# Kernel tuning notes

Hardware: AMD Instinct MI355X
Metric: run time of the kernel (lower is better)

The kernel has to match this reference:

```python
import jax, jax.numpy as jnp
import numpy as np
import math

B, S, D = 2, 4096, 512
H, DH = 8, 64
L = 128            # num_landmarks
W = 128            # window_size
EXT = W // 2       # 64
WIN = 2 * EXT + W  # 256
G = S // W         # 32 chunks
EPS = 1e-5


def _ln(x, g, b):
    mu = jnp.mean(x, axis=-1, keepdims=True)
    var = jnp.mean((x - mu) ** 2, axis=-1, keepdims=True)
    return (x - mu) * jax.lax.rsqrt(var + EPS) * g + b


def setup_inputs() -> dict:
    key = jax.random.key(0)
    ks = jax.random.split(key, 12)
    sd = 1.0 / math.sqrt(D)
    inp = {
        "X": jax.random.normal(ks[0], (B, S, D), dtype=jnp.float32),
        "mask": jnp.ones((B, S), dtype=jnp.int32),
        "Wq": jax.random.normal(ks[1], (D, H * DH), dtype=jnp.float32) * sd,
        "bq": jnp.zeros((H * DH,), jnp.float32),
        "Wk": jax.random.normal(ks[2], (D, H * DH), dtype=jnp.float32) * sd,
        "bk": jnp.zeros((H * DH,), jnp.float32),
        "Wv": jax.random.normal(ks[3], (D, H * DH), dtype=jnp.float32) * sd,
        "bv": jnp.zeros((H * DH,), jnp.float32),
        "Wo": jax.random.normal(ks[4], (H * DH, D), dtype=jnp.float32) * sd,
        "bo": jnp.zeros((D,), jnp.float32),
        "ln_l_g": jnp.ones((H * DH,), jnp.float32),
        "ln_l_b": jnp.zeros((H * DH,), jnp.float32),
        "ln_s_g": jnp.ones((H * DH,), jnp.float32),
        "ln_s_b": jnp.zeros((H * DH,), jnp.float32),
        "Wd": jax.random.normal(ks[5], (D, H * L), dtype=jnp.float32) * sd,
        "bd": jnp.zeros((H * L,), jnp.float32),
    }
    return inp


def reference(X, mask, Wq, bq, Wk, bk, Wv, bv, Wo, bo,
              ln_l_g, ln_l_b, ln_s_g, ln_s_b, Wd, bd):
    scale = 1.0 / math.sqrt(DH)

    def split(x):  # [B,S,H*DH] -> [B,H,S,DH]
        return x.reshape(B, S, H, DH).transpose(0, 2, 1, 3)

    Q = split(X @ Wq + bq) * scale
    K = split(_ln(X @ Wk + bk, ln_l_g, ln_l_b))
    V = split(_ln(X @ Wv + bv, ln_l_g, ln_l_b))
    pad_mask = (mask == 0)  # True = padding, [B,S]

    # ---- landmark compression branch ----
    hs = jax.nn.softmax((X @ Wd + bd).astype(jnp.float32), axis=1)  # over seq
    hs = hs.astype(X.dtype).reshape(B, S, H, L).transpose(0, 2, 3, 1)  # [B,H,L,S]
    Kc = jnp.einsum('bhls,bhsd->bhld', hs, K)
    Vc = jnp.einsum('bhls,bhsd->bhld', hs, V)
    # dual_ln_s over full model dim
    Kc = _ln(Kc.transpose(0, 2, 1, 3).reshape(B, L, H * DH), ln_s_g, ln_s_b)
    Kc = Kc.reshape(B, L, H, DH).transpose(0, 2, 1, 3)
    Vc = _ln(Vc.transpose(0, 2, 1, 3).reshape(B, L, H * DH), ln_s_g, ln_s_b)
    Vc = Vc.reshape(B, L, H, DH).transpose(0, 2, 1, 3)

    attn_c = jnp.einsum('bhqd,bhld->bhql', Q, Kc)  # [B,H,S,L]

    # ---- sliding-window branch (v2 tiling) ----
    idx = jnp.arange(G)[:, None] * W + jnp.arange(WIN)[None, :]
    K_pad = jnp.pad(K, ((0, 0), (0, 0), (EXT, EXT), (0, 0)))
    K_tiles = K_pad[:, :, idx, :]
    Qt = Q.reshape(B, H, G, W, DH)
    win_scores = jnp.einsum('bhgqd,bhgkd->bhgqk', Qt, K_tiles)
    mask_pad = jnp.pad(pad_mask, ((0, 0), (EXT, EXT)), constant_values=True)
    mask_tiles = mask_pad[:, idx]
    win_scores = jnp.where(mask_tiles[:, None, :, None, :], -jnp.inf, win_scores)
    win_scores = win_scores.reshape(B, H, S, WIN)

    # ---- joint softmax over [landmarks | window] ----
    all_scores = jnp.concatenate([attn_c, win_scores], axis=-1)
    all_attn = jax.nn.softmax(all_scores.astype(jnp.float32), axis=-1).astype(X.dtype)
    all_attn = jnp.where(pad_mask[:, None, :, None], 0.0, all_attn)

    C = jnp.einsum('bhql,bhld->bhqd', all_attn[..., :L], Vc)
    wp = all_attn[..., L:].reshape(B, H, G, W, WIN)
    V_pad = jnp.pad(V, ((0, 0), (0, 0), (EXT, EXT), (0, 0)))
    V_tiles = V_pad[:, :, idx, :]
    C = C + jnp.einsum('bhgqk,bhgkd->bhgqd', wp, V_tiles).reshape(B, H, S, DH)

    out = C.transpose(0, 2, 1, 3).reshape(B, S, H * DH) @ Wo + bo
    return out
```

## Files before the change

kernel.cpp:

```cpp
#include <hip/hip_runtime.h>
#include <hip/hip_bf16.h>

#define S_LEN 4096
#define Hn 8
#define DHn 64
#define Lc 128
#define HL 1024
#define KD 512

typedef __attribute__((ext_vector_type(8))) short bshort8;
typedef __attribute__((ext_vector_type(4))) float f32x4;

__device__ __forceinline__ short f2bs(float f) {
    union { float f; unsigned u; } x; x.f = f;
    const unsigned r = x.u + 0x7FFFu + ((x.u >> 16) & 1u);
    return (short)(r >> 16);
}
__device__ __forceinline__ float bs2f(short s) {
    union { unsigned u; float f; } x; x.u = ((unsigned)(unsigned short)s) << 16;
    return x.f;
}

__device__ __forceinline__ void gl16(const short* g, short* l) {
    __builtin_amdgcn_global_load_lds((const __attribute__((address_space(1))) void*)g,
                                     (__attribute__((address_space(3))) void*)l, 16, 0, 0);
}

__global__ __launch_bounds__(256) void prep_all(const float* __restrict__ X,
    const float* __restrict__ Wq, const float* __restrict__ Wk, const float* __restrict__ Wv,
    const float* __restrict__ Wd, const float* __restrict__ Wo,
    short* __restrict__ Xbf, short* __restrict__ WTall, short* __restrict__ WoT)
{
    const int t = threadIdx.x;
    int blk = blockIdx.x;
    if (blk < 2048) {
        const int i = (blk * 256 + t) * 8;
        const float4 a = *(const float4*)&X[i];
        const float4 b = *(const float4*)&X[i + 4];
        bshort8 o;
        o[0] = f2bs(a.x); o[1] = f2bs(a.y); o[2] = f2bs(a.z); o[3] = f2bs(a.w);
        o[4] = f2bs(b.x); o[5] = f2bs(b.y); o[6] = f2bs(b.z); o[7] = f2bs(b.w);
        *(bshort8*)&Xbf[i] = o;
        return;
    }
    blk -= 2048;
    const float* W; short* out; int N;
    if (blk < 256)       { W = Wq; out = WTall;              N = 512;  }
    else if (blk < 512)  { W = Wk; out = WTall + 512 * 512;  N = 512;  blk -= 256; }
    else if (blk < 768)  { W = Wv; out = WTall + 1024 * 512; N = 512;  blk -= 512; }
    else if (blk < 1280) { W = Wd; out = WTall + 1536 * 512; N = 1024; blk -= 768; }
    else                 { W = Wo; out = WoT;                N = 512;  blk -= 1280; }
    const int nb = N >> 5;
    const int n0 = (blk % nb) * 32, k0 = (blk / nb) * 32;
    __shared__ float Tl[32][33];
    const int tx = t & 31, ty = t >> 5;
#pragma unroll
    for (int i = ty; i < 32; i += 8)
        Tl[i][tx] = W[(size_t)(k0 + i) * N + n0 + tx];
    __syncthreads();
#pragma unroll
    for (int i = ty; i < 32; i += 8)
        out[(size_t)(n0 + i) * KD + k0 + tx] = f2bs(Tl[tx][i]);
}

__global__ __launch_bounds__(256) void gemm_proj(const short* __restrict__ Xbf,
    const short* __restrict__ WT,
    const float* __restrict__ bq, const float* __restrict__ bk,
    const float* __restrict__ bv, const float* __restrict__ bd,
    short* __restrict__ Qbf, short* __restrict__ KbBf, short* __restrict__ VbBf,
    short* __restrict__ DlogBf)
{
    __shared__ __align__(16) short A_s[128 * 32];
    __shared__ __align__(16) short B_s[128 * 32];
    const int t = threadIdx.x;
    const int n0 = blockIdx.x * 128, m0 = blockIdx.y * 128;
    const int lane = t & 63, wave = t >> 6;
    const int wm = wave >> 1, wn = wave & 1;
    const int quad = lane >> 4, r15 = lane & 15;
    const int eOff = t * 8;
    const int am = eOff >> 5, ak = eOff & 31;
    f32x4 acc[4][4];
#pragma unroll
    for (int i = 0; i < 4; ++i)
#pragma unroll
        for (int j = 0; j < 4; ++j) acc[i][j] = (f32x4){0.f, 0.f, 0.f, 0.f};

    for (int kk = 0; kk < KD; kk += 32) {
        gl16(&Xbf[(size_t)(m0 + am) * KD + kk + ak],      &A_s[eOff]);
        gl16(&Xbf[(size_t)(m0 + 64 + am) * KD + kk + ak], &A_s[2048 + eOff]);
        gl16(&WT[(size_t)(n0 + am) * KD + kk + ak],       &B_s[eOff]);
        gl16(&WT[(size_t)(n0 + 64 + am) * KD + kk + ak],  &B_s[2048 + eOff]);
        __syncthreads();
        bshort8 af[4], bfr[4];
#pragma unroll
        for (int i = 0; i < 4; ++i) af[i]  = *(const bshort8*)&A_s[(wm * 64 + i * 16 + r15) * 32 + quad * 8];
#pragma unroll
        for (int j = 0; j < 4; ++j) bfr[j] = *(const bshort8*)&B_s[(wn * 64 + j * 16 + r15) * 32 + quad * 8];
#pragma unroll
        for (int i = 0; i < 4; ++i)
#pragma unroll
            for (int j = 0; j < 4; ++j)
                acc[i][j] = __builtin_amdgcn_mfma_f32_16x16x32_bf16(af[i], bfr[j], acc[i][j], 0, 0, 0);
        __syncthreads();
    }
    const int seg = (n0 >= 1536) ? 3 : (n0 >> 9);
#pragma unroll
    for (int i = 0; i < 4; ++i)
#pragma unroll
        for (int j = 0; j < 4; ++j)
#pragma unroll
            for (int r = 0; r < 4; ++r) {
                const int gm = m0 + wm * 64 + i * 16 + quad * 4 + r;
                const int gn = n0 + wn * 64 + j * 16 + r15;
                float v = acc[i][j][r];
                if (seg == 0) {
                    v = (v + bq[gn]) * 0.125f;
                    const int bb = gm >> 12, s = gm & 4095, hh = gn >> 6, d = gn & 63;
                    Qbf[((size_t)(bb * Hn + hh) * S_LEN + s) * DHn + d] = f2bs(v);
                } else if (seg == 1) {
                    KbBf[(size_t)gm * 512 + (gn - 512)] = f2bs(v + bk[gn - 512]);
                } else if (seg == 2) {
                    VbBf[(size_t)gm * 512 + (gn - 1024)] = f2bs(v + bv[gn - 1024]);
                } else {
                    DlogBf[(size_t)gm * 1024 + (gn - 1536)] = f2bs(v + bd[gn - 1536]);
                }
            }
}

__global__ __launch_bounds__(256) void gemm_out(const short* __restrict__ Abf,
    const short* __restrict__ WT, const float* __restrict__ bias, float* __restrict__ outp)
{
    __shared__ __align__(16) short A_s[64 * 32];
    __shared__ __align__(16) short B_s[64 * 32];
    const int t = threadIdx.x;
    const int n0 = blockIdx.x * 64, m0 = blockIdx.y * 64;
    const int lane = t & 63, wave = t >> 6;
    const int quad = lane >> 4, r15 = lane & 15;
    const int eOff = t * 8;
    const int am = eOff >> 5, ak = eOff & 31;
    f32x4 acc[4];
#pragma unroll
    for (int j = 0; j < 4; ++j) acc[j] = (f32x4){0.f, 0.f, 0.f, 0.f};

    for (int kk = 0; kk < KD; kk += 32) {
        gl16(&Abf[(size_t)(m0 + am) * KD + kk + ak], &A_s[eOff]);
        gl16(&WT[(size_t)(n0 + am) * KD + kk + ak],  &B_s[eOff]);
        __syncthreads();
        const bshort8 af = *(const bshort8*)&A_s[(wave * 16 + r15) * 32 + quad * 8];
#pragma unroll
        for (int j = 0; j < 4; ++j) {
            const bshort8 bfr = *(const bshort8*)&B_s[(j * 16 + r15) * 32 + quad * 8];
            acc[j] = __builtin_amdgcn_mfma_f32_16x16x32_bf16(af, bfr, acc[j], 0, 0, 0);
        }
        __syncthreads();
    }
#pragma unroll
    for (int j = 0; j < 4; ++j)
#pragma unroll
        for (int r = 0; r < 4; ++r) {
            const int gm = m0 + wave * 16 + quad * 4 + r;
            const int gn = n0 + j * 16 + r15;
            outp[(size_t)gm * 512 + gn] = acc[j][r] + bias[gn];
        }
}

__global__ __launch_bounds__(256) void ln_ip(const short* __restrict__ KbBf, const short* __restrict__ VbBf,
    const float* __restrict__ g, const float* __restrict__ beta,
    short* __restrict__ Kbf, short* __restrict__ Vbf)
{
    const short* src = blockIdx.y ? VbBf : KbBf;
    short* dst = blockIdx.y ? Vbf : Kbf;
    const int row = blockIdx.x, t = threadIdx.x;
    const size_t base = (size_t)row * 512;
    const float x0 = bs2f(src[base + t]);
    const float x1 = bs2f(src[base + t + 256]);
    float s = x0 + x1, ss = x0 * x0 + x1 * x1;
#pragma unroll
    for (int off = 32; off >= 1; off >>= 1) { s += __shfl_xor(s, off); ss += __shfl_xor(ss, off); }
    __shared__ float red[2][4];
    if ((t & 63) == 0) { red[0][t >> 6] = s; red[1][t >> 6] = ss; }
    __syncthreads();
    s = red[0][0] + red[0][1] + red[0][2] + red[0][3];
    ss = red[1][0] + red[1][1] + red[1][2] + red[1][3];
    const float mu = s * (1.f / 512.f);
    const float r = rsqrtf(ss * (1.f / 512.f) - mu * mu + 1e-5f);
    const int bb = row >> 12, sidx = row & 4095;
#pragma unroll
    for (int half = 0; half < 2; ++half) {
        const int c = t + half * 256;
        const float x = half ? x1 : x0;
        const float v = (x - mu) * r * g[c] + beta[c];
        dst[((size_t)(bb * Hn + (c >> 6)) * S_LEN + sidx) * DHn + (c & 63)] = f2bs(v);
    }
}

__global__ __launch_bounds__(256) void kcvc_mfma(const short* __restrict__ Dlog,
    const short* __restrict__ Kbf, const short* __restrict__ Vbf,
    short* __restrict__ partK, short* __restrict__ partV, float* __restrict__ partZ)
{
    __shared__ __align__(16) short aa[128 * 72];
    __shared__ __align__(16) short Kt[64 * 72];
    __shared__ __align__(16) short Vt[64 * 72];
    __shared__ float zsh[256];
    const int t = threadIdx.x;
    const int seg = blockIdx.x, h = blockIdx.y, b = blockIdx.z;
    const int s0 = seg * 128;
    const size_t bh = (size_t)(b * Hn + h);
    const int lane = t & 63, wave = t >> 6;
    const int quad = lane >> 4, r15 = lane & 15;
    const int al = t & 127, ah = t >> 7;
    const int vj = t & 63, vd0 = (t >> 6) * 16;
    float zacc = 0.f;
    f32x4 aK[2][4], aV[2][4];
#pragma unroll
    for (int i = 0; i < 2; ++i)
#pragma unroll
        for (int j = 0; j < 4; ++j) { aK[i][j] = (f32x4){0.f,0.f,0.f,0.f}; aV[i][j] = (f32x4){0.f,0.f,0.f,0.f}; }

    for (int c = 0; c < 2; ++c) {
        const int sc0 = s0 + c * 64;
        if (c) __syncthreads();
#pragma unroll
        for (int gch = 0; gch < 4; ++gch) {
            bshort8 o;
#pragma unroll
            for (int j = 0; j < 8; ++j) {
                const int s = sc0 + ah * 32 + gch * 8 + j;
                const float e = __expf(bs2f(Dlog[((size_t)b * S_LEN + s) * HL + h * Lc + al]));
                zacc += e;
                o[j] = f2bs(e);
            }
            *(bshort8*)&aa[al * 72 + ah * 32 + gch * 8] = o;
        }
        {
            const size_t rb = (bh * S_LEN + sc0 + vj) * DHn + vd0;
            const bshort8 k0 = *(const bshort8*)&Kbf[rb];
            const bshort8 k1 = *(const bshort8*)&Kbf[rb + 8];
            const bshort8 v0 = *(const bshort8*)&Vbf[rb];
            const bshort8 v1 = *(const bshort8*)&Vbf[rb + 8];
#pragma unroll
            for (int i = 0; i < 8; ++i) {
                Kt[(vd0 + i) * 72 + vj] = k0[i]; Kt[(vd0 + 8 + i) * 72 + vj] = k1[i];
                Vt[(vd0 + i) * 72 + vj] = v0[i]; Vt[(vd0 + 8 + i) * 72 + vj] = v1[i];
            }
        }
        __syncthreads();
#pragma unroll
        for (int ks = 0; ks < 2; ++ks) {
            const bshort8 a0 = *(const bshort8*)&aa[(wave * 32 + r15) * 72 + ks * 32 + quad * 8];
            const bshort8 a1 = *(const bshort8*)&aa[(wave * 32 + 16 + r15) * 72 + ks * 32 + quad * 8];
#pragma unroll
            for (int j = 0; j < 4; ++j) {
                const bshort8 bk = *(const bshort8*)&Kt[(j * 16 + r15) * 72 + ks * 32 + quad * 8];
                const bshort8 bv = *(const bshort8*)&Vt[(j * 16 + r15) * 72 + ks * 32 + quad * 8];
                aK[0][j] = __builtin_amdgcn_mfma_f32_16x16x32_bf16(a0, bk, aK[0][j], 0, 0, 0);
                aK[1][j] = __builtin_amdgcn_mfma_f32_16x16x32_bf16(a1, bk, aK[1][j], 0, 0, 0);
                aV[0][j] = __builtin_amdgcn_mfma_f32_16x16x32_bf16(a0, bv, aV[0][j], 0, 0, 0);
                aV[1][j] = __builtin_amdgcn_mfma_f32_16x16x32_bf16(a1, bv, aV[1][j], 0, 0, 0);
            }
        }
    }
    zsh[t] = zacc;
    __syncthreads();
    if (t < 128)
        partZ[((size_t)(bh * Lc + t)) * 32 + seg] = zsh[t] + zsh[t + 128];
#pragma unroll
    for (int i = 0; i < 2; ++i)
#pragma unroll
        for (int j = 0; j < 4; ++j)
#pragma unroll
            for (int r = 0; r < 4; ++r) {
                const int l = wave * 32 + i * 16 + quad * 4 + r;
                const int d = j * 16 + r15;
                const size_t o = (((size_t)(b * Lc + l)) * 32 + seg) * 512 + h * 64 + d;
                partK[o] = f2bs(aK[i][j][r]);
                partV[o] = f2bs(aV[i][j][r]);
            }
}

__global__ __launch_bounds__(256) void kcvc_s2(const short* __restrict__ partK,
    const short* __restrict__ partV, const float* __restrict__ partZ,
    const float* __restrict__ g, const float* __restrict__ beta,
    short* __restrict__ KcBf, short* __restrict__ VcBf)
{
    const int l = blockIdx.x, b = blockIdx.y, t = threadIdx.x;
    __shared__ float zh[8];
    if (t < 8) {
        float z = 0.f;
        const size_t zb = ((size_t)((b * Hn + t) * Lc + l)) * 32;
#pragma unroll
        for (int seg = 0; seg < 32; ++seg) z += partZ[zb + seg];
        zh[t] = 1.f / z;
    }
    const size_t base = ((size_t)(b * Lc + l)) * 32 * 512;
    float k0 = 0.f, k1 = 0.f, v0 = 0.f, v1 = 0.f;
    for (int ch = 0; ch < 32; ++ch) {
        const size_t o = base + (size_t)ch * 512;
        k0 += bs2f(partK[o + t]);       k1 += bs2f(partK[o + t + 256]);
        v0 += bs2f(partV[o + t]);       v1 += bs2f(partV[o + t + 256]);
    }
    __syncthreads();
    const float z0 = zh[t >> 6], z1 = zh[(t + 256) >> 6];
    k0 *= z0; k1 *= z1; v0 *= z0; v1 *= z1;
    float sk = k0 + k1, ssk = k0 * k0 + k1 * k1;
    float sv = v0 + v1, ssv = v0 * v0 + v1 * v1;
#pragma unroll
    for (int off = 32; off >= 1; off >>= 1) {
        sk += __shfl_xor(sk, off); ssk += __shfl_xor(ssk, off);
        sv += __shfl_xor(sv, off); ssv += __shfl_xor(ssv, off);
    }
    __shared__ float red[4][4];
    if ((t & 63) == 0) {
        red[0][t >> 6] = sk; red[1][t >> 6] = ssk;
        red[2][t >> 6] = sv; red[3][t >> 6] = ssv;
    }
    __syncthreads();
    sk = red[0][0] + red[0][1] + red[0][2] + red[0][3];
    ssk = red[1][0] + red[1][1] + red[1][2] + red[1][3];
    sv = red[2][0] + red[2][1] + red[2][2] + red[2][3];
    ssv = red[3][0] + red[3][1] + red[3][2] + red[3][3];
    const float muK = sk * (1.f / 512.f);
    const float rK = rsqrtf(ssk * (1.f / 512.f) - muK * muK + 1e-5f);
    const float muV = sv * (1.f / 512.f);
    const float rV = rsqrtf(ssv * (1.f / 512.f) - muV * muV + 1e-5f);
#pragma unroll
    for (int half = 0; half < 2; ++half) {
        const int c = t + half * 256;
        const float xk = half ? k1 : k0;
        const float xv = half ? v1 : v0;
        const size_t o = ((size_t)(b * Hn + (c >> 6)) * Lc + l) * DHn + (c & 63);
        KcBf[o] = f2bs((xk - muK) * rK * g[c] + beta[c]);
        VcBf[o] = f2bs((xv - muV) * rV * g[c] + beta[c]);
    }
}

__global__ __launch_bounds__(256) void attn_mfma(
    const short* __restrict__ Qbf, const short* __restrict__ Kbf, const short* __restrict__ Vbf,
    const short* __restrict__ KcBf, const short* __restrict__ VcBf,
    const int* __restrict__ mask, short* __restrict__ C)
{
    __shared__ __align__(16) short Q_l[128 * 72];
    __shared__ __align__(16) short K_l[64 * 72];
    __shared__ __align__(16) short Vt_l[64 * 72];
    __shared__ __align__(16) short P_l[128 * 72];
    __shared__ float vb[64];
    const int t = threadIdx.x;
    const int qt = blockIdx.x, h = blockIdx.y, b = blockIdx.z;
    const int q0 = qt * 128;
    const size_t bh = (size_t)(b * Hn + h);
    const int lane = t & 63, wave = t >> 6;
    const int quad = lane >> 4, r15 = lane & 15;
    const int sr = t >> 2, sc = (t & 3) * 16;
    const int vj = t & 63, vd0 = (t >> 6) * 16;

#pragma unroll
    for (int r = 0; r < 2; ++r) {
        const int row = r * 64 + sr;
        const size_t gq = (bh * S_LEN + q0 + row) * DHn + sc;
        const bshort8 a = *(const bshort8*)&Qbf[gq];
        const bshort8 b8 = *(const bshort8*)&Qbf[gq + 8];
        *(bshort8*)&Q_l[row * 72 + sc] = a;
        *(bshort8*)&Q_l[row * 72 + sc + 8] = b8;
    }
    f32x4 o[2][4];
#pragma unroll
    for (int i = 0; i < 2; ++i)
#pragma unroll
        for (int df = 0; df < 4; ++df) o[i][df] = (f32x4){0.f, 0.f, 0.f, 0.f};
    float lrow[2][4] = {{0.f, 0.f, 0.f, 0.f}, {0.f, 0.f, 0.f, 0.f}};

    for (int cc = 0; cc < 6; ++cc) {
        const short* ksrc; const short* vsrc;
        int sk0 = 0;
        if (cc < 2) {
            ksrc = &KcBf[(bh * Lc + cc * 64) * DHn];
            vsrc = &VcBf[(bh * Lc + cc * 64) * DHn];
        } else {
            sk0 = q0 - 64 + (cc - 2) * 64;
            if (sk0 < 0 || sk0 >= S_LEN) continue;
            ksrc = &Kbf[(bh * S_LEN + sk0) * DHn];
            vsrc = &Vbf[(bh * S_LEN + sk0) * DHn];
        }
        __syncthreads();
        if (t < 64) {
            float v = 0.f;
            if (cc >= 2 && mask[b * S_LEN + sk0 + t] == 0) v = -1e30f;
            vb[t] = v;
        }
        {
            const bshort8 a = *(const bshort8*)&ksrc[sr * 64 + sc];
            const bshort8 b8 = *(const bshort8*)&ksrc[sr * 64 + sc + 8];
            *(bshort8*)&K_l[sr * 72 + sc] = a;
            *(bshort8*)&K_l[sr * 72 + sc + 8] = b8;
        }
        {
            const bshort8 v0 = *(const bshort8*)&vsrc[vj * 64 + vd0];
            const bshort8 v1 = *(const bshort8*)&vsrc[vj * 64 + vd0 + 8];
#pragma unroll
            for (int i = 0; i < 8; ++i) {
                Vt_l[(vd0 + i) * 72 + vj] = v0[i];
                Vt_l[(vd0 + 8 + i) * 72 + vj] = v1[i];
            }
        }
        __syncthreads();
        f32x4 c[2][4];
#pragma unroll
        for (int i = 0; i < 2; ++i)
#pragma unroll
            for (int jf = 0; jf < 4; ++jf) c[i][jf] = (f32x4){0.f, 0.f, 0.f, 0.f};
#pragma unroll
        for (int ks = 0; ks < 2; ++ks) {
            bshort8 aq[2];
#pragma unroll
            for (int i = 0; i < 2; ++i)
                aq[i] = *(const bshort8*)&Q_l[(wave * 32 + i * 16 + r15) * 72 + ks * 32 + quad * 8];
#pragma unroll
            for (int jf = 0; jf < 4; ++jf) {
                const bshort8 bk = *(const bshort8*)&K_l[(jf * 16 + r15) * 72 + ks * 32 + quad * 8];
                c[0][jf] = __builtin_amdgcn_mfma_f32_16x16x32_bf16(aq[0], bk, c[0][jf], 0, 0, 0);
                c[1][jf] = __builtin_amdgcn_mfma_f32_16x16x32_bf16(aq[1], bk, c[1][jf], 0, 0, 0);
            }
        }
        float vbl[4];
#pragma unroll
        for (int jf = 0; jf < 4; ++jf) vbl[jf] = vb[jf * 16 + r15];
        float sum[2][4] = {{0.f, 0.f, 0.f, 0.f}, {0.f, 0.f, 0.f, 0.f}};
#pragma unroll
        for (int i = 0; i < 2; ++i)
#pragma unroll
            for (int jf = 0; jf < 4; ++jf)
#pragma unroll
                for (int r = 0; r < 4; ++r) {
                    const float p = __expf(c[i][jf][r] + vbl[jf]);
                    sum[i][r] += p;
                    P_l[(wave * 32 + i * 16 + quad * 4 + r) * 72 + jf * 16 + r15] = f2bs(p);
                }
#pragma unroll
        for (int off = 1; off <= 8; off <<= 1)
#pragma unroll
            for (int i = 0; i < 2; ++i)
#pragma unroll
                for (int r = 0; r < 4; ++r) sum[i][r] += __shfl_xor(sum[i][r], off);
#pragma unroll
        for (int i = 0; i < 2; ++i)
#pragma unroll
            for (int r = 0; r < 4; ++r) lrow[i][r] += sum[i][r];
#pragma unroll
        for (int ks = 0; ks < 2; ++ks) {
            bshort8 ap[2];
#pragma unroll
            for (int i = 0; i < 2; ++i)
                ap[i] = *(const bshort8*)&P_l[(wave * 32 + i * 16 + r15) * 72 + ks * 32 + quad * 8];
#pragma unroll
            for (int df = 0; df < 4; ++df) {
                const bshort8 bv = *(const bshort8*)&Vt_l[(df * 16 + r15) * 72 + ks * 32 + quad * 8];
                o[0][df] = __builtin_amdgcn_mfma_f32_16x16x32_bf16(ap[0], bv, o[0][df], 0, 0, 0);
                o[1][df] = __builtin_amdgcn_mfma_f32_16x16x32_bf16(ap[1], bv, o[1][df], 0, 0, 0);
            }
        }
    }
#pragma unroll
    for (int i = 0; i < 2; ++i)
#pragma unroll
        for (int r = 0; r < 4; ++r) {
            const int q = q0 + wave * 32 + i * 16 + quad * 4 + r;
            const float rl = (mask[b * S_LEN + q] == 0) ? 0.f : (1.f / lrow[i][r]);
            const size_t ob = ((size_t)b * S_LEN + q) * 512 + h * 64;
#pragma unroll
            for (int df = 0; df < 4; ++df)
                C[ob + df * 16 + r15] = f2bs(o[i][df][r] * rl);
        }
}

extern "C" void kernel_launch(void* const* d_in, const int* in_sizes, int n_in,
                              void* d_out, int out_size, void* d_ws, size_t ws_size,
                              hipStream_t stream) {
    (void)in_sizes; (void)n_in; (void)out_size; (void)ws_size;
    const float* X    = (const float*)d_in[0];
    const int*   mask = (const int*)d_in[1];
    const float* Wq = (const float*)d_in[2];  const float* bq = (const float*)d_in[3];
    const float* Wk = (const float*)d_in[4];  const float* bk = (const float*)d_in[5];
    const float* Wv = (const float*)d_in[6];  const float* bv = (const float*)d_in[7];
    const float* Wo = (const float*)d_in[8];  const float* bo = (const float*)d_in[9];
    const float* lnlg = (const float*)d_in[10]; const float* lnlb = (const float*)d_in[11];
    const float* lnsg = (const float*)d_in[12]; const float* lnsb = (const float*)d_in[13];
    const float* Wd = (const float*)d_in[14]; const float* bd = (const float*)d_in[15];

    short* sw = (short*)d_ws;
    short* Qbf    = sw;
    short* Kbf    = Qbf + 4194304;
    short* Vbf    = Kbf + 4194304;
    short* KbBf   = Vbf + 4194304;
    short* VbBf   = KbBf + 4194304;
    short* DlogBf = VbBf + 4194304;
    short* Xbf    = DlogBf + 8388608;
    short* WTall  = Xbf + 4194304;
    short* WoT    = WTall + 1310720;
    short* KcBf   = WoT + 262144;
    short* VcBf   = KcBf + 131072;
    short* partV  = VcBf + 131072;
    float* partZ  = (float*)(partV + 4194304);
    short* partK  = Xbf;
    short* Cbf    = Xbf;

    const dim3 blk(256);
    prep_all<<<3584, blk, 0, stream>>>(X, Wq, Wk, Wv, Wd, Wo, Xbf, WTall, WoT);
    gemm_proj<<<dim3(20, 64), blk, 0, stream>>>(Xbf, WTall, bq, bk, bv, bd, Qbf, KbBf, VbBf, DlogBf);
    ln_ip<<<dim3(8192, 2), blk, 0, stream>>>(KbBf, VbBf, lnlg, lnlb, Kbf, Vbf);
    kcvc_mfma<<<dim3(32, 8, 2), blk, 0, stream>>>(DlogBf, Kbf, Vbf, partK, partV, partZ);
    kcvc_s2<<<dim3(128, 2), blk, 0, stream>>>(partK, partV, partZ, lnsg, lnsb, KcBf, VcBf);
    attn_mfma<<<dim3(32, 8, 2), blk, 0, stream>>>(Qbf, Kbf, Vbf, KcBf, VcBf, mask, Cbf);
    gemm_out<<<dim3(8, 128), blk, 0, stream>>>(Cbf, WoT, bo, (float*)d_out);
}
```

Baseline: 220.9 us.

## Remap GEMM block order for XCD locality, widen out-proj tile, split kcvc_s2 by K/V

The projection and output GEMMs now use a 1D grid whose block index is remapped so that consecutive blocks landing on the same XCD (id & 7) share output column tiles, aiming to improve L2 reuse of weight and activation tiles. The output GEMM tile is widened from 64x64 to 64x128, giving each wave 8 accumulators and halving redundant A loads at the cost of more registers and fewer blocks. kcvc_s2 is split across a z-dimension so K and V are normalized by separate blocks, doubling parallelism for that small reduction kernel but recomputing the Z normalizers twice.

Measured after the change: 210.7 us. -4.6%, faster.

```diff
diff --git a/kernel.cpp b/kernel.cpp
--- a/kernel.cpp
+++ b/kernel.cpp
@@ -73,7 +73,10 @@
     __shared__ __align__(16) short A_s[128 * 32];
     __shared__ __align__(16) short B_s[128 * 32];
     const int t = threadIdx.x;
-    const int n0 = blockIdx.x * 128, m0 = blockIdx.y * 128;
+    const int id = blockIdx.x;
+    const int x8 = id & 7, j8 = id >> 3;
+    const int m0 = (x8 * 8 + (j8 & 7)) * 128;
+    const int n0 = (j8 >> 3) * 128;
     const int lane = t & 63, wave = t >> 6;
     const int wm = wave >> 1, wn = wave & 1;
     const int quad = lane >> 4, r15 = lane & 15;
@@ -131,31 +134,35 @@
     const short* __restrict__ WT, const float* __restrict__ bias, float* __restrict__ outp)
 {
     __shared__ __align__(16) short A_s[64 * 32];
-    __shared__ __align__(16) short B_s[64 * 32];
+    __shared__ __align__(16) short B_s[128 * 32];
     const int t = threadIdx.x;
-    const int n0 = blockIdx.x * 64, m0 = blockIdx.y * 64;
+    const int id = blockIdx.x;
+    const int x8 = id & 7, j8 = id >> 3;
+    const int m0 = (x8 * 16 + (j8 & 15)) * 64;
+    const int n0 = (j8 >> 4) * 128;
     const int lane = t & 63, wave = t >> 6;
     const int quad = lane >> 4, r15 = lane & 15;
     const int eOff = t * 8;
     const int am = eOff >> 5, ak = eOff & 31;
-    f32x4 acc[4];
-#pragma unroll
-    for (int j = 0; j < 4; ++j) acc[j] = (f32x4){0.f, 0.f, 0.f, 0.f};
+    f32x4 acc[8];
+#pragma unroll
+    for (int j = 0; j < 8; ++j) acc[j] = (f32x4){0.f, 0.f, 0.f, 0.f};
 
     for (int kk = 0; kk < KD; kk += 32) {
-        gl16(&Abf[(size_t)(m0 + am) * KD + kk + ak], &A_s[eOff]);
-        gl16(&WT[(size_t)(n0 + am) * KD + kk + ak],  &B_s[eOff]);
+        gl16(&Abf[(size_t)(m0 + am) * KD + kk + ak],      &A_s[eOff]);
+        gl16(&WT[(size_t)(n0 + am) * KD + kk + ak],       &B_s[eOff]);
+        gl16(&WT[(size_t)(n0 + 64 + am) * KD + kk + ak],  &B_s[2048 + eOff]);
         __syncthreads();
         const bshort8 af = *(const bshort8*)&A_s[(wave * 16 + r15) * 32 + quad * 8];
 #pragma unroll
-        for (int j = 0; j < 4; ++j) {
+        for (int j = 0; j < 8; ++j) {
             const bshort8 bfr = *(const bshort8*)&B_s[(j * 16 + r15) * 32 + quad * 8];
             acc[j] = __builtin_amdgcn_mfma_f32_16x16x32_bf16(af, bfr, acc[j], 0, 0, 0);
         }
         __syncthreads();
     }
 #pragma unroll
-    for (int j = 0; j < 4; ++j)
+    for (int j = 0; j < 8; ++j)
 #pragma unroll
         for (int r = 0; r < 4; ++r) {
             const int gm = m0 + wave * 16 + quad * 4 + r;
@@ -284,6 +291,8 @@
     short* __restrict__ KcBf, short* __restrict__ VcBf)
 {
     const int l = blockIdx.x, b = blockIdx.y, t = threadIdx.x;
+    const short* part = blockIdx.z ? partV : partK;
+    short* dst = blockIdx.z ? VcBf : KcBf;
     __shared__ float zh[8];
     if (t < 8) {
         float z = 0.f;
@@ -293,44 +302,33 @@
         zh[t] = 1.f / z;
     }
     const size_t base = ((size_t)(b * Lc + l)) * 32 * 512;
-    float k0 = 0.f, k1 = 0.f, v0 = 0.f, v1 = 0.f;
+    float k0 = 0.f, k1 = 0.f;
     for (int ch = 0; ch < 32; ++ch) {
         const size_t o = base + (size_t)ch * 512;
-        k0 += bs2f(partK[o + t]);       k1 += bs2f(partK[o + t + 256]);
-        v0 += bs2f(partV[o + t]);       v1 += bs2f(partV[o + t + 256]);
+        k0 += bs2f(part[o + t]);
+        k1 += bs2f(part[o + t + 256]);
     }
     __syncthreads();
     const float z0 = zh[t >> 6], z1 = zh[(t + 256) >> 6];
-    k0 *= z0; k1 *= z1; v0 *= z0; v1 *= z1;
+    k0 *= z0; k1 *= z1;
     float sk = k0 + k1, ssk = k0 * k0 + k1 * k1;
-    float sv = v0 + v1, ssv = v0 * v0 + v1 * v1;
 #pragma unroll
     for (int off = 32; off >= 1; off >>= 1) {
         sk += __shfl_xor(sk, off); ssk += __shfl_xor(ssk, off);
-        sv += __shfl_xor(sv, off); ssv += __shfl_xor(ssv, off);
-    }
-    __shared__ float red[4][4];
-    if ((t & 63) == 0) {
-        red[0][t >> 6] = sk; red[1][t >> 6] = ssk;
-        red[2][t >> 6] = sv; red[3][t >> 6] = ssv;
-    }
+    }
+    __shared__ float red[2][4];
+    if ((t & 63) == 0) { red[0][t >> 6] = sk; red[1][t >> 6] = ssk; }
     __syncthreads();
     sk = red[0][0] + red[0][1] + red[0][2] + red[0][3];
     ssk = red[1][0] + red[1][1] + red[1][2] + red[1][3];
-    sv = red[2][0] + red[2][1] + red[2][2] + red[2][3];
-    ssv = red[3][0] + red[3][1] + red[3][2] + red[3][3];
-    const float muK = sk * (1.f / 512.f);
-    const float rK = rsqrtf(ssk * (1.f / 512.f) - muK * muK + 1e-5f);
-    const float muV = sv * (1.f / 512.f);
-    const float rV = rsqrtf(ssv * (1.f / 512.f) - muV * muV + 1e-5f);
+    const float mu = sk * (1.f / 512.f);
+    const float r = rsqrtf(ssk * (1.f / 512.f) - mu * mu + 1e-5f);
 #pragma unroll
     for (int half = 0; half < 2; ++half) {
         const int c = t + half * 256;
         const float xk = half ? k1 : k0;
-        const float xv = half ? v1 : v0;
         const size_t o = ((size_t)(b * Hn + (c >> 6)) * Lc + l) * DHn + (c & 63);
-        KcBf[o] = f2bs((xk - muK) * rK * g[c] + beta[c]);
-        VcBf[o] = f2bs((xv - muV) * rV * g[c] + beta[c]);
+        dst[o] = f2bs((xk - mu) * r * g[c] + beta[c]);
     }
 }
 
@@ -505,10 +503,10 @@
 
     const dim3 blk(256);
     prep_all<<<3584, blk, 0, stream>>>(X, Wq, Wk, Wv, Wd, Wo, Xbf, WTall, WoT);
-    gemm_proj<<<dim3(20, 64), blk, 0, stream>>>(Xbf, WTall, bq, bk, bv, bd, Qbf, KbBf, VbBf, DlogBf);
+    gemm_proj<<<1280, blk, 0, stream>>>(Xbf, WTall, bq, bk, bv, bd, Qbf, KbBf, VbBf, DlogBf);
     ln_ip<<<dim3(8192, 2), blk, 0, stream>>>(KbBf, VbBf, lnlg, lnlb, Kbf, Vbf);
     kcvc_mfma<<<dim3(32, 8, 2), blk, 0, stream>>>(DlogBf, Kbf, Vbf, partK, partV, partZ);
-    kcvc_s2<<<dim3(128, 2), blk, 0, stream>>>(partK, partV, partZ, lnsg, lnsb, KcBf, VcBf);
+    kcvc_s2<<<dim3(128, 2, 2), blk, 0, stream>>>(partK, partV, partZ, lnsg, lnsb, KcBf, VcBf);
     attn_mfma<<<dim3(32, 8, 2), blk, 0, stream>>>(Qbf, Kbf, Vbf, KcBf, VcBf, mask, Cbf);
-    gemm_out<<<dim3(8, 128), blk, 0, stream>>>(Cbf, WoT, bo, (float*)d_out);
-}
+    gemm_out<<<512, blk, 0, stream>>>(Cbf, WoT, bo, (float*)d_out);
+}
```
